# Optimization experiments

Measured on AMD Instinct MI355X. Metric: run time of the kernel, lower is better.

The kernel has to match this reference:

```python
import jax, jax.numpy as jnp
import numpy as np

B, N, S, K = 8, 4096, 1024, 16
C_IN, C_OUT = 128, 256
BN_EPS = 1e-5


def setup_inputs() -> dict:
    key = jax.random.key(0)
    ks = jax.random.split(key, 20)
    sc = 0.02
    p = {
        'xyz': jax.random.normal(ks[0], (B, N, 3), jnp.float32),
        'points': jax.random.normal(ks[1], (B, N, C_IN), jnp.float32),
        'wq': jax.random.normal(ks[2], (C_IN, C_OUT), jnp.float32) * sc,
        'wk': jax.random.normal(ks[3], (C_IN, C_OUT), jnp.float32) * sc,
        'wv': jax.random.normal(ks[4], (C_IN, C_OUT), jnp.float32) * sc,
        'dw1': jax.random.normal(ks[5], (3, C_OUT), jnp.float32) * sc,
        'db1': jnp.zeros((C_OUT,), jnp.float32),
        'dw2': jax.random.normal(ks[6], (C_OUT, C_OUT), jnp.float32) * sc,
        'db2': jnp.zeros((C_OUT,), jnp.float32),
        'gw1': jax.random.normal(ks[7], (C_OUT, C_OUT), jnp.float32) * sc,
        'gb1': jnp.zeros((C_OUT,), jnp.float32),
        'gw2': jax.random.normal(ks[8], (C_OUT, C_OUT), jnp.float32) * sc,
        'gb2': jnp.zeros((C_OUT,), jnp.float32),
        'lw': jax.random.normal(ks[9], (C_OUT, C_OUT), jnp.float32) * sc,
        'lb': jnp.zeros((C_OUT,), jnp.float32),
        'bn_g': jnp.ones((C_OUT,), jnp.float32),
        'bn_b': jnp.zeros((C_OUT,), jnp.float32),
    }
    return p


def _fps(xyz, npoint):
    # xyz: [N,3] -> farthest point sample indices [npoint] (deterministic start at 0,
    # matching torch impl with fixed seed semantics)
    n = xyz.shape[0]
    def step(carry, _):
        dist, far = carry
        centroid = xyz[far]                      # [3]
        d = jnp.sum((xyz - centroid) ** 2, -1)   # [N]
        dist = jnp.minimum(dist, d)
        return (dist, jnp.argmax(dist).astype(jnp.int32)), far
    init = (jnp.full((n,), 1e10, xyz.dtype), jnp.int32(0))
    _, idx = jax.lax.scan(step, init, None, length=npoint)
    return idx  # [npoint]


def _mlp2(x, w1, b1, w2, b2):
    return jax.nn.relu(x @ w1 + b1) @ w2 + b2


def reference(xyz, points, wq, wk, wv, dw1, db1, dw2, db2,
              gw1, gb1, gw2, gb2, lw, lb, bn_g, bn_b):
    # --- sample_and_group (FPS + KNN, knn=True) ---
    fps_idx = jax.vmap(lambda x: _fps(x, S))(xyz)                 # [B,S]
    new_xyz = jnp.take_along_axis(xyz, fps_idx[..., None], 1)     # [B,S,3]
    # squared distances sampled->all: [B,S,N]
    d2 = (jnp.sum(new_xyz**2, -1)[:, :, None]
          - 2.0 * jnp.einsum('bsc,bnc->bsn', new_xyz, xyz)
          + jnp.sum(xyz**2, -1)[:, None, :])
    knn_idx = jax.lax.top_k(-d2, K)[1]                            # [B,S,K]
    gather = jax.vmap(lambda a, i: a[i])
    knn_xyz = gather(xyz, knn_idx)                                # [B,S,K,3]
    knn_xyz_norm = knn_xyz - new_xyz[:, :, None]                  # centered coords
    knn_points = gather(points, knn_idx)                          # [B,S,K,C_in]
    sampled_points = jnp.take_along_axis(points, fps_idx[..., None], 1)  # [B,S,C_in]

    # --- vector attention ---
    q = sampled_points @ wq                                       # [B,S,C_out]
    k = knn_points @ wk                                           # [B,S,K,C_out]
    v = knn_points @ wv                                           # [B,S,K,C_out]
    pos_enc = _mlp2(knn_xyz_norm, dw1, db1, dw2, db2)             # [B,S,K,C_out]
    att = _mlp2(q[:, :, None] - k + pos_enc, gw1, gb1, gw2, gb2)  # [B,S,K,C_out]
    att = jax.nn.softmax(att / np.sqrt(C_OUT).astype(np.float32), axis=-2)
    res = jnp.einsum('bmnf,bmnf->bmf', att, v + pos_enc)          # [B,S,C_out]

    # --- fc_last + BatchNorm1d (training-mode batch stats, biased var) + ReLU ---
    res = res @ lw + lb
    mean = jnp.mean(res, axis=(0, 1))
    var = jnp.var(res, axis=(0, 1))
    res = bn_g * (res - mean) * jax.lax.rsqrt(var + BN_EPS) + bn_b
    res = jax.nn.relu(res)
    return new_xyz, res
```

## Files before the change

### kernel.cpp

```cpp
#include <hip/hip_runtime.h>

typedef unsigned long long ull;
typedef __attribute__((ext_vector_type(8))) short bf16x8;
typedef __attribute__((ext_vector_type(4))) float f32x4;

__device__ __forceinline__ unsigned short bf16b(float x){
    unsigned u = __float_as_uint(x);
    unsigned r = (u + 0x7FFFu + ((u >> 16) & 1u)) >> 16;
    return (unsigned short)r;
}
__device__ __forceinline__ float b2f(unsigned short u){
    return __uint_as_float(((unsigned)u) << 16);
}
__device__ __forceinline__ void st4(unsigned short* p, f32x4 v){
    ull pk = (ull)bf16b(v[0]) | (((ull)bf16b(v[1])) << 16)
           | (((ull)bf16b(v[2])) << 32) | (((ull)bf16b(v[3])) << 48);
    *(ull*)p = pk;
}
__device__ __forceinline__ f32x4 ld4(const unsigned short* p){
    ull pk = *(const ull*)p;
    f32x4 v;
    v[0] = b2f((unsigned short)pk);
    v[1] = b2f((unsigned short)(pk >> 16));
    v[2] = b2f((unsigned short)(pk >> 32));
    v[3] = b2f((unsigned short)(pk >> 48));
    return v;
}

#define DPPMAX(k, ctrl) do { \
    unsigned _lo = (unsigned)(k), _hi = (unsigned)((k) >> 32); \
    unsigned _l2 = (unsigned)__builtin_amdgcn_update_dpp((int)_lo, (int)_lo, (ctrl), 0xF, 0xF, false); \
    unsigned _h2 = (unsigned)__builtin_amdgcn_update_dpp((int)_hi, (int)_hi, (ctrl), 0xF, 0xF, false); \
    ull _k2 = (((ull)_h2) << 32) | _l2; \
    if (_k2 > (k)) (k) = _k2; \
} while (0)
#define DPPMIN(k, ctrl) do { \
    unsigned _lo = (unsigned)(k), _hi = (unsigned)((k) >> 32); \
    unsigned _l2 = (unsigned)__builtin_amdgcn_update_dpp((int)_lo, (int)_lo, (ctrl), 0xF, 0xF, false); \
    unsigned _h2 = (unsigned)__builtin_amdgcn_update_dpp((int)_hi, (int)_hi, (ctrl), 0xF, 0xF, false); \
    ull _k2 = (((ull)_h2) << 32) | _l2; \
    if (_k2 < (k)) (k) = _k2; \
} while (0)

template<int KT>
__device__ __forceinline__ int swz(int r, int c){
    return r * (KT * 32) + ((((c >> 3) + r) & (KT * 4 - 1)) << 3) + (c & 7);
}

template<int KT>
__device__ __forceinline__ void gemmT(const unsigned short* __restrict__ Wt,
                                      const unsigned short* __restrict__ Blds,
                                      int ch0, int lane, f32x4 acc[4][4])
{
    int i = lane & 15, q = lane >> 4;
#pragma unroll
    for (int kt = 0; kt < KT; kt++){
        int k0 = kt * 32 + q * 8;
        bf16x8 bfr[4], afr[4];
#pragma unroll
        for (int nt = 0; nt < 4; nt++)
            bfr[nt] = *(const bf16x8*)(Blds + swz<KT>(nt * 16 + i, k0));
#pragma unroll
        for (int mt = 0; mt < 4; mt++)
            afr[mt] = *(const bf16x8*)(Wt + (size_t)(ch0 + mt * 16 + i) * (KT * 32) + k0);
#pragma unroll
        for (int mt = 0; mt < 4; mt++)
#pragma unroll
            for (int nt = 0; nt < 4; nt++)
                acc[mt][nt] = __builtin_amdgcn_mfma_f32_16x16x32_bf16(afr[mt], bfr[nt], acc[mt][nt], 0, 0, 0);
    }
}

#define ZERO44(A) do { _Pragma("unroll") for (int _m = 0; _m < 4; _m++) \
    { _Pragma("unroll") for (int _n = 0; _n < 4; _n++) { A[_m][_n][0]=0.f;A[_m][_n][1]=0.f;A[_m][_n][2]=0.f;A[_m][_n][3]=0.f; } } } while(0)

#define CTRL_AUX   (8 << 4)

__device__ __forceinline__ int ald(const int* p){
    return __hip_atomic_load(p, __ATOMIC_RELAXED, __HIP_MEMORY_SCOPE_AGENT);
}
__device__ __forceinline__ void ast(int* p, int v){
    __hip_atomic_store(p, v, __ATOMIC_RELAXED, __HIP_MEMORY_SCOPE_AGENT);
}

__device__ __forceinline__ void knn_one(int t2, int G, float qx, float qy, float qz,
        const float* __restrict__ xyz,
        int* __restrict__ knn_idx, float* d2s, ull* kslot)
{
    int b = G >> 10;
    int lane = t2 & 63, wvi = t2 >> 6;
    float qq = qx * qx + qy * qy + qz * qz;
    for (int j = 0; j < 16; j++){
        int p = t2 + (j << 8);
        const float* s = xyz + ((size_t)b * 4096 + p) * 3;
        float x = s[0], y = s[1], z = s[2];
        d2s[p] = qq - 2.f * (qx * x + qy * y + qz * z) + (x * x + y * y + z * z);
    }
    __syncthreads();
    for (int r = 0; r < 16; r++){
        ull best = ~0ull;
#pragma unroll
        for (int j = 0; j < 16; j++){
            int p = t2 + (j << 8);
            unsigned bb = __float_as_uint(d2s[p]);
            bb = (bb & 0x80000000u) ? ~bb : (bb | 0x80000000u);
            ull key = (((ull)bb) << 32) | (unsigned)p;
            if (key < best) best = key;
        }
        DPPMIN(best, 0xB1); DPPMIN(best, 0x4E); DPPMIN(best, 0x141);
        DPPMIN(best, 0x140); DPPMIN(best, 0x142); DPPMIN(best, 0x143);
        if (lane == 63) kslot[wvi] = best;
        __syncthreads();
        if (t2 == 0){
            ull bk = kslot[0];
            for (int w = 1; w < 4; w++) if (kslot[w] < bk) bk = kslot[w];
            int p = (int)(unsigned)bk;
            knn_idx[(size_t)G * 16 + r] = p;
            d2s[p] = 3.0e38f;
        }
        __syncthreads();
    }
}

__device__ void attn_unit(int t, char* base, int G0, const float* nxL4,
    const unsigned short* __restrict__ pts16,
    const float* __restrict__ xyz,
    const int* __restrict__ knn_idx, const float* __restrict__ qbuf,
    const unsigned short* __restrict__ wkT, const unsigned short* __restrict__ wvT,
    const unsigned short* __restrict__ dw2T, const unsigned short* __restrict__ gw1T,
    const unsigned short* __restrict__ gw2T,
    const float* __restrict__ dw1, const float* __restrict__ db1,
    const float* __restrict__ db2, const float* __restrict__ gb1, const float* __restrict__ gb2,
    unsigned short* __restrict__ resY)
{
    unsigned short* bufA = (unsigned short*)base;
    unsigned short* bufU = (unsigned short*)(base + 32768);
    int lane = t & 63, wave = t >> 6;
    int i = lane & 15, q = lane >> 4;
    int ch0 = wave * 64;
    unsigned short* ptsA = bufU;
    float* dw1s  = (float*)(bufU + 8192);
    float* db1s  = (float*)(bufU + 9728);
    float* xyznS = (float*)(bufU + 10240);
    int*   idxs  = (int*)  (bufU + 10624);

    if (t < 64) idxs[t] = knn_idx[G0 * 16 + t];
    dw1s[t] = dw1[t]; dw1s[256 + t] = dw1[256 + t]; dw1s[512 + t] = dw1[512 + t];
    db1s[t] = db1[t];
    __syncthreads();

    if (t < 64){
        int G = G0 + (t >> 4); int bb = G >> 10; int p = idxs[t];
        const float* xp = xyz + ((size_t)bb * 4096 + p) * 3;
        const float* nz = nxL4 + (t >> 4) * 3;
        xyznS[t * 3 + 0] = xp[0] - nz[0];
        xyznS[t * 3 + 1] = xp[1] - nz[1];
        xyznS[t * 3 + 2] = xp[2] - nz[2];
    }
    {
        int r = t >> 2, seg = t & 3;
        int G = G0 + (r >> 4); int bb = G >> 10; int p = idxs[r];
        const uint4* src = (const uint4*)(pts16 + ((size_t)bb * 4096 + p) * 128 + seg * 32);
#pragma unroll
        for (int j = 0; j < 4; j++){
            uint4 v = src[j];
            *(uint4*)(ptsA + swz<4>(r, seg * 32 + j * 8)) = v;
        }
    }
    __syncthreads();

    {
        int r = lane;
        int o0 = wave * 64;
        float x = xyznS[r * 3], y = xyznS[r * 3 + 1], z = xyznS[r * 3 + 2];
#pragma unroll
        for (int j = 0; j < 64; j += 4){
            int o = o0 + j;
            f32x4 v;
#pragma unroll
            for (int e = 0; e < 4; e++)
                v[e] = fmaxf(db1s[o + e] + x * dw1s[o + e] + y * dw1s[256 + o + e] + z * dw1s[512 + o + e], 0.f);
            st4(bufA + swz<8>(r, o), v);
        }
    }
    __syncthreads();

    f32x4 accP[4][4]; ZERO44(accP);
    gemmT<8>(dw2T, bufA, ch0, lane, accP);
#pragma unroll
    for (int mt = 0; mt < 4; mt++){
        f32x4 d2v = *(const f32x4*)(db2 + ch0 + mt * 16 + q * 4);
#pragma unroll
        for (int nt = 0; nt < 4; nt++) accP[mt][nt] += d2v;
    }
    f32x4 accK[4][4]; ZERO44(accK);
    gemmT<4>(wkT, ptsA, ch0, lane, accK);
    __syncthreads();

#pragma unroll
    for (int mt = 0; mt < 4; mt++){
        int c = ch0 + mt * 16 + q * 4;
#pragma unroll
        for (int nt = 0; nt < 4; nt++){
            int r = nt * 16 + i;
            f32x4 qv = *(const f32x4*)(qbuf + (size_t)(G0 + nt) * 256 + c);
            f32x4 tv = qv - accK[mt][nt] + accP[mt][nt];
            st4(bufA + swz<8>(r, c), tv);
        }
    }
    f32x4 accV[4][4]; ZERO44(accV);
    gemmT<4>(wvT, ptsA, ch0, lane, accV);
    __syncthreads();

#pragma unroll
    for (int mt = 0; mt < 4; mt++){
        int c = ch0 + mt * 16 + q * 4;
#pragma unroll
        for (int nt = 0; nt < 4; nt++){
            int r = nt * 16 + i;
            f32x4 uv = accV[mt][nt] + accP[mt][nt];
            st4(bufU + swz<8>(r, c), uv);
        }
    }
    f32x4 acc1[4][4]; ZERO44(acc1);
    gemmT<8>(gw1T, bufA, ch0, lane, acc1);
    __syncthreads();

#pragma unroll
    for (int mt = 0; mt < 4; mt++){
        int c = ch0 + mt * 16 + q * 4;
        f32x4 g1v = *(const f32x4*)(gb1 + c);
#pragma unroll
        for (int nt = 0; nt < 4; nt++){
            int r = nt * 16 + i;
            f32x4 av = acc1[mt][nt] + g1v;
#pragma unroll
            for (int e = 0; e < 4; e++) av[e] = fmaxf(av[e], 0.f);
            st4(bufA + swz<8>(r, c), av);
        }
    }
    __syncthreads();

    f32x4 acc2[4][4]; ZERO44(acc2);
    gemmT<8>(gw2T, bufA, ch0, lane, acc2);
    __syncthreads();

#pragma unroll
    for (int mt = 0; mt < 4; mt++){
        int c = ch0 + mt * 16 + q * 4;
        f32x4 g2v = *(const f32x4*)(gb2 + c);
#pragma unroll
        for (int nt = 0; nt < 4; nt++){
            int r = nt * 16 + i;
            f32x4 ev;
#pragma unroll
            for (int e = 0; e < 4; e++) ev[e] = __expf((acc2[mt][nt][e] + g2v[e]) * 0.0625f);
            st4(bufA + swz<8>(r, c), ev);
        }
    }
    __syncthreads();

    {
        int g = t >> 6, c4 = (t & 63) * 4;
        f32x4 num; num[0]=0.f;num[1]=0.f;num[2]=0.f;num[3]=0.f;
        f32x4 den = num;
#pragma unroll
        for (int rr = 0; rr < 16; rr++){
            int r = g * 16 + rr;
            f32x4 e4 = ld4(bufA + swz<8>(r, c4));
            f32x4 u4 = ld4(bufU + swz<8>(r, c4));
            num += e4 * u4;
            den += e4;
        }
        f32x4 rv = num / den;
        st4(resY + (size_t)(G0 + g) * 256 + c4, rv);
    }
}

__device__ void do_chunk(int t, int c, char* SM,
    const float* __restrict__ xyz, const float* __restrict__ nxyz,
    const float* __restrict__ points, const float* __restrict__ wqT,
    const int* __restrict__ fps_idx, int* __restrict__ knn_idx, float* __restrict__ qbuf,
    const unsigned short* __restrict__ pts16,
    const unsigned short* __restrict__ wkT, const unsigned short* __restrict__ wvT,
    const unsigned short* __restrict__ dw2T, const unsigned short* __restrict__ gw1T,
    const unsigned short* __restrict__ gw2T,
    const float* __restrict__ dw1, const float* __restrict__ db1,
    const float* __restrict__ db2, const float* __restrict__ gb1, const float* __restrict__ gb2,
    unsigned short* __restrict__ resY)
{
    int g0 = c * 8;
    int sub = t >> 8, t2 = t & 255;
    int*   fpsL = (int*)  (SM + 131200);
    float* nxL  = (float*)(SM + 131232);
    if (t < 64){
        for (;;){
            int v = 0; bool ok = true;
            if (t < 8){
                v = ald(fps_idx + g0 + t); ok = (v != -1);
            } else if (t < 32){
                v = ald((const int*)nxyz + (size_t)g0 * 3 + (t - 8)); ok = (v != (int)0xFFFFFFFF);
            }
            if (__ballot(ok) == ~0ull){
                if (t < 8) fpsL[t] = v;
                else if (t < 32) ((int*)nxL)[t - 8] = v;
                break;
            }
            __builtin_amdgcn_s_sleep(8);
        }
    }
    __syncthreads();
    float* d2s = (float*)(SM + sub * 16384);
    ull* kslot = (ull*)(SM + 131072) + sub * 4;
    for (int r4 = 0; r4 < 4; r4++){
        int gl = r4 * 2 + sub;
        knn_one(t2, g0 + gl, nxL[gl * 3], nxL[gl * 3 + 1], nxL[gl * 3 + 2],
                xyz, knn_idx, d2s, kslot);
    }
    __syncthreads();
    {
        float* sp = (float*)SM;
        if (t < 256){
            int r = t >> 5, c4 = (t & 31) * 4;
            int G = g0 + r; int b = G >> 10; int p = fpsL[r];
            *(f32x4*)(sp + r * 128 + c4) = *(const f32x4*)(points + ((size_t)b * 4096 + p) * 128 + c4);
        }
        __syncthreads();
        float acc[4] = {0.f, 0.f, 0.f, 0.f};
        const float* wr = wqT + t2 * 128;
        for (int k = 0; k < 128; k += 4){
            f32x4 w = *(const f32x4*)(wr + k);
#pragma unroll
            for (int r = 0; r < 4; r++){
                const float* row = sp + (sub * 4 + r) * 128;
                acc[r] += w[0]*row[k] + w[1]*row[k+1] + w[2]*row[k+2] + w[3]*row[k+3];
            }
        }
#pragma unroll
        for (int r = 0; r < 4; r++) qbuf[(size_t)(g0 + sub * 4 + r) * 256 + t2] = acc[r];
        __syncthreads();
    }
    attn_unit(t2, SM + sub * 65536, g0 + sub * 4, nxL + sub * 12, pts16, xyz, knn_idx, qbuf,
              wkT, wvT, dw2T, gw1T, gw2T, dw1, db1, db2, gb1, gb2, resY);
    __syncthreads();
}

__global__ __launch_bounds__(256) void init_ws(int* __restrict__ ctrl,
                                               int* __restrict__ fps_idx,
                                               int* __restrict__ nxyz_i)
{
    int i = blockIdx.x * 256 + threadIdx.x;
    if (i < 256) ctrl[i] = 0;
    if (i < 8192) fps_idx[i] = -1;
    if (i < 24576) nxyz_i[i] = (int)0xFFFFFFFF;
}

__global__ __launch_bounds__(512, 2) void mega(
    const float* __restrict__ xyz, float* __restrict__ nxyz_out, int* __restrict__ fps_idx,
    const float* __restrict__ pts, unsigned short* __restrict__ pts16,
    const float* __restrict__ wq, const float* __restrict__ wk, const float* __restrict__ wv,
    const float* __restrict__ dw2, const float* __restrict__ gw1, const float* __restrict__ gw2,
    const float* __restrict__ lw,
    float* __restrict__ wqT, unsigned short* __restrict__ wkT, unsigned short* __restrict__ wvT,
    unsigned short* __restrict__ dw2T, unsigned short* __restrict__ gw1T,
    unsigned short* __restrict__ gw2T, unsigned short* __restrict__ lwT,
    float* __restrict__ stats,
    const float* __restrict__ dw1, const float* __restrict__ db1, const float* __restrict__ db2,
    const float* __restrict__ gb1, const float* __restrict__ gb2,
    int* __restrict__ knn_idx, float* __restrict__ qbuf, unsigned short* __restrict__ resY,
    int* __restrict__ ctrl)
{
    __shared__ __align__(16) char SM[132096];
    int blk = blockIdx.x, t = threadIdx.x;

    if (blk < 8){
        int b = blk;
        int lane = t & 63, wvi = t >> 6;
        float* sx = (float*)SM;
        float* sy = (float*)(SM + 16384);
        float* sz = (float*)(SM + 32768);
        int* farS = (int*)(SM + 49152);
        ull (*slotK)[8] = (ull(*)[8])(SM + 53248);
        for (int p = t; p < 4096; p += 512){
            const float* s = xyz + ((size_t)b * 4096 + p) * 3;
            sx[p] = s[0]; sy[p] = s[1]; sz[p] = s[2];
        }
        __syncthreads();
        float px[8], py[8], pz[8], dist[8];
        unsigned nplo[8];
#pragma unroll
        for (int j = 0; j < 8; j++){
            int p = t + (j << 9);
            px[j] = sx[p]; py[j] = sy[p]; pz[j] = sz[p];
            dist[j] = 1e10f;
            nplo[j] = ~(unsigned)p;
            asm volatile("" : "+v"(px[j]), "+v"(py[j]), "+v"(pz[j]), "+v"(nplo[j]));
        }
        int far = 0;
        float cx = sx[0], cy = sy[0], cz = sz[0];
        int par = 0;
        for (int s = 0; s < 1024; s++){
            if (t == 0) farS[s] = far;
            ull lb = 0;
#pragma unroll
            for (int j = 0; j < 8; j++){
                float dx = __fsub_rn(px[j], cx);
                float dy = __fsub_rn(py[j], cy);
                float dz = __fsub_rn(pz[j], cz);
                float d = __fadd_rn(__fadd_rn(__fmul_rn(dx, dx), __fmul_rn(dy, dy)), __fmul_rn(dz, dz));
                float nd = fminf(dist[j], d);
                dist[j] = nd;
                ull k2 = (((ull)__float_as_uint(nd)) << 32) | nplo[j];
                if (k2 > lb) lb = k2;
            }
            DPPMAX(lb, 0xB1); DPPMAX(lb, 0x4E); DPPMAX(lb, 0x141);
            DPPMAX(lb, 0x140); DPPMAX(lb, 0x142); DPPMAX(lb, 0x143);
            if (lane == 63) slotK[par][wvi] = lb;
            __syncthreads();
            ull k = slotK[par][lane & 7];
            DPPMAX(k, 0xB1); DPPMAX(k, 0x4E); DPPMAX(k, 0x141);
            far = (int)(~(unsigned)k);
            cx = sx[far]; cy = sy[far]; cz = sz[far];
            if (((s & 15) == 15) && wvi == 7){
                int s0 = s - 15;
                if (lane < 16){
                    ast(fps_idx + b * 1024 + s0 + lane, farS[s0 + lane]);
                } else {
                    int idx = lane - 16;
                    int st = s0 + idx / 3, d = idx - (idx / 3) * 3;
                    int f = farS[st];
                    float v = (d == 0) ? sx[f] : ((d == 1) ? sy[f] : sz[f]);
                    ast((int*)nxyz_out + (size_t)b * 3072 + st * 3 + d, __float_as_int(v));
                }
            }
            par ^= 1;
        }
        if (t == 0){ while (ald(ctrl + CTRL_AUX) < 248) __builtin_amdgcn_s_sleep(16); }
        __syncthreads();
        __threadfence();
        do_chunk(t, b * 128 + 127, SM, xyz, nxyz_out, pts, wqT, fps_idx, knn_idx, qbuf,
                 pts16, wkT, wvT, dw2T, gw1T, gw2T, dw1, db1, db2, gb1, gb2, resY);
        return;
    }

    int w = blk - 8;
    for (int base = w; base < 704; base += 248){
        if (base == 0) stats[t & 511] = 0.f;
        int i = base * 512 + t;
        if (i < 32768){ int n = i >> 7, kk = i & 127; wqT[i] = wq[kk * 256 + n]; }
        else if (i < 65536){ int j = i - 32768; int n = j >> 7, kk = j & 127; wkT[j] = bf16b(wk[kk * 256 + n]); }
        else if (i < 98304){ int j = i - 65536; int n = j >> 7, kk = j & 127; wvT[j] = bf16b(wv[kk * 256 + n]); }
        else if (i < 163840){ int j = i - 98304; int n = j >> 8, kk = j & 255; dw2T[j] = bf16b(dw2[kk * 256 + n]); }
        else if (i < 229376){ int j = i - 163840; int n = j >> 8, kk = j & 255; gw1T[j] = bf16b(gw1[kk * 256 + n]); }
        else if (i < 294912){ int j = i - 229376; int n = j >> 8, kk = j & 255; gw2T[j] = bf16b(gw2[kk * 256 + n]); }
        else { int j = i - 294912; int n = j >> 8, kk = j & 255; lwT[j] = bf16b(lw[kk * 256 + n]); }
    }
    for (int base = w; base < 2048; base += 248){
        int i = (base * 512 + t) * 4;
        f32x4 v = *(const f32x4*)(pts + i);
        ull pk = (ull)bf16b(v[0]) | (((ull)bf16b(v[1])) << 16)
               | (((ull)bf16b(v[2])) << 32) | (((ull)bf16b(v[3])) << 48);
        *(ull*)(pts16 + i) = pk;
    }
    __threadfence();
    __syncthreads();
    if (t == 0){
        atomicAdd(ctrl + CTRL_AUX, 1);
        while (ald(ctrl + CTRL_AUX) < 248) __builtin_amdgcn_s_sleep(16);
    }
    __syncthreads();
    __threadfence();
    for (int j = 0; j < 5; j++){
        int p = w + 248 * j;
        if (p >= 1016) break;
        int bb = p & 7, cc = p >> 3;
        do_chunk(t, bb * 128 + cc, SM, xyz, nxyz_out, pts, wqT, fps_idx, knn_idx, qbuf,
                 pts16, wkT, wvT, dw2T, gw1T, gw2T, dw1, db1, db2, gb1, gb2, resY);
    }
}

__global__ __launch_bounds__(256, 2) void z_gemm(const unsigned short* __restrict__ resY,
                                                 const unsigned short* __restrict__ lwT,
                                                 const float* __restrict__ lb,
                                                 float* __restrict__ zbuf,
                                                 float* __restrict__ stats)
{
    int t = threadIdx.x, lane = t & 63, wave = t >> 6;
    int i = lane & 15, q = lane >> 4;
    int row0 = blockIdx.x * 128;
    int ch0 = wave * 64;
    f32x4 acc[4][8];
#pragma unroll
    for (int mt = 0; mt < 4; mt++)
#pragma unroll
        for (int nt = 0; nt < 8; nt++){ acc[mt][nt][0]=0.f;acc[mt][nt][1]=0.f;acc[mt][nt][2]=0.f;acc[mt][nt][3]=0.f; }
#pragma unroll
    for (int kt = 0; kt < 8; kt++){
        int k0 = kt * 32 + q * 8;
        bf16x8 a[4], bb[8];
#pragma unroll
        for (int mt = 0; mt < 4; mt++)
            a[mt] = *(const bf16x8*)(lwT + (size_t)(ch0 + mt * 16 + i) * 256 + k0);
#pragma unroll
        for (int nt = 0; nt < 8; nt++)
            bb[nt] = *(const bf16x8*)(resY + (size_t)(row0 + nt * 16 + i) * 256 + k0);
#pragma unroll
        for (int mt = 0; mt < 4; mt++)
#pragma unroll
            for (int nt = 0; nt < 8; nt++)
                acc[mt][nt] = __builtin_amdgcn_mfma_f32_16x16x32_bf16(a[mt], bb[nt], acc[mt][nt], 0, 0, 0);
    }
    f32x4 s1[4], s2[4];
#pragma unroll
    for (int mt = 0; mt < 4; mt++){ s1[mt][0]=0.f;s1[mt][1]=0.f;s1[mt][2]=0.f;s1[mt][3]=0.f; s2[mt]=s1[mt]; }
#pragma unroll
    for (int mt = 0; mt < 4; mt++){
        int c = ch0 + mt * 16 + q * 4;
        f32x4 lb4 = *(const f32x4*)(lb + c);
#pragma unroll
        for (int nt = 0; nt < 8; nt++){
            int r = row0 + nt * 16 + i;
            f32x4 z = acc[mt][nt] + lb4;
            *(f32x4*)(zbuf + (size_t)r * 256 + c) = z;
            s1[mt] += z;
            s2[mt] += z * z;
        }
    }
    for (int m = 1; m < 16; m <<= 1){
#pragma unroll
        for (int mt = 0; mt < 4; mt++)
#pragma unroll
            for (int e = 0; e < 4; e++){
                s1[mt][e] += __shfl_xor(s1[mt][e], m);
                s2[mt][e] += __shfl_xor(s2[mt][e], m);
            }
    }
    if (i == 0){
#pragma unroll
        for (int mt = 0; mt < 4; mt++){
            int c = ch0 + mt * 16 + q * 4;
#pragma unroll
            for (int e = 0; e < 4; e++){
                atomicAdd(&stats[c + e], s1[mt][e]);
                atomicAdd(&stats[256 + c + e], s2[mt][e]);
            }
        }
    }
}

__global__ __launch_bounds__(256) void bn_kernel(const float* __restrict__ zbuf,
                                                 const float* __restrict__ stats,
                                                 const float* __restrict__ bn_g,
                                                 const float* __restrict__ bn_b,
                                                 float* __restrict__ out)
{
    int G = blockIdx.x, c = threadIdx.x;
    float mean = stats[c] * (1.f / 8192.f);
    float var = stats[256 + c] * (1.f / 8192.f) - mean * mean;
    float inv = rsqrtf(var + 1e-5f);
    float z = zbuf[(size_t)G * 256 + c];
    float y = bn_g[c] * (z - mean) * inv + bn_b[c];
    out[24576 + (size_t)G * 256 + c] = fmaxf(y, 0.f);
}

extern "C" void kernel_launch(void* const* d_in, const int* in_sizes, int n_in,
                              void* d_out, int out_size, void* d_ws, size_t ws_size,
                              hipStream_t stream)
{
    const float* xyz    = (const float*)d_in[0];
    const float* points = (const float*)d_in[1];
    const float* wq  = (const float*)d_in[2];
    const float* wk  = (const float*)d_in[3];
    const float* wv  = (const float*)d_in[4];
    const float* dw1 = (const float*)d_in[5];
    const float* db1 = (const float*)d_in[6];
    const float* dw2 = (const float*)d_in[7];
    const float* db2 = (const float*)d_in[8];
    const float* gw1 = (const float*)d_in[9];
    const float* gb1 = (const float*)d_in[10];
    const float* gw2 = (const float*)d_in[11];
    const float* gb2 = (const float*)d_in[12];
    const float* lw  = (const float*)d_in[13];
    const float* lb  = (const float*)d_in[14];
    const float* bn_g = (const float*)d_in[15];
    const float* bn_b = (const float*)d_in[16];
    float* out = (float*)d_out;

    char* ws = (char*)d_ws;
    int*            fps_idx = (int*)(ws + 0);
    int*            knn_idx = (int*)(ws + 32768);
    float*          qbuf    = (float*)(ws + 557056);
    unsigned short* pts16   = (unsigned short*)(ws + 8945664);
    unsigned short* wkT     = (unsigned short*)(ws + 17334272);
    unsigned short* wvT     = (unsigned short*)(ws + 17399808);
    unsigned short* dw2T    = (unsigned short*)(ws + 17465344);
    unsigned short* gw1T    = (unsigned short*)(ws + 17596416);
    unsigned short* gw2T    = (unsigned short*)(ws + 17727488);
    unsigned short* lwT     = (unsigned short*)(ws + 17858560);
    float*          wqT     = (float*)(ws + 17989632);
    unsigned short* resY    = (unsigned short*)(ws + 18120704);
    float*          zbuf    = (float*)(ws + 22315008);
    float*          stats   = (float*)(ws + 30703616);
    int*            ctrl    = (int*)(ws + 22315008);

    init_ws<<<96, 256, 0, stream>>>(ctrl, fps_idx, (int*)out);
    mega<<<256, 512, 0, stream>>>(xyz, out, fps_idx, points, pts16,
                                  wq, wk, wv, dw2, gw1, gw2, lw,
                                  wqT, wkT, wvT, dw2T, gw1T, gw2T, lwT, stats,
                                  dw1, db1, db2, gb1, gb2,
                                  knn_idx, qbuf, resY, ctrl);
    z_gemm<<<64, 256, 0, stream>>>(resY, lwT, lb, zbuf, stats);
    bn_kernel<<<8192, 256, 0, stream>>>(zbuf, stats, bn_g, bn_b, out);
}
```

Measured before the change: 926.4 us.

## Keep KNN distances in registers and double-buffer wave-min slots to halve barriers

The KNN top-16 selection now keeps each thread's 16 candidate distance keys in registers instead of shared memory. It also caches a per-thread local minimum that only the owning thread recomputes after its point is selected. Every thread reduces the four per-wave minima itself, and the slots alternate between two buffers, so one of the two block barriers per selection round is dropped. This cuts LDS traffic and repeated 16-element rescans, at the cost of more registers and a wider kslot region (8 entries per sub-group, 128 bytes total) that must not overlap fpsL at offset 131200.

```diff
diff --git a/kernel.cpp b/kernel.cpp
--- a/kernel.cpp
+++ b/kernel.cpp
@@ -85,40 +85,52 @@
 
 __device__ __forceinline__ void knn_one(int t2, int G, float qx, float qy, float qz,
         const float* __restrict__ xyz,
-        int* __restrict__ knn_idx, float* d2s, ull* kslot)
+        int* __restrict__ knn_idx, ull* kslot )
 {
     int b = G >> 10;
     int lane = t2 & 63, wvi = t2 >> 6;
     float qq = qx * qx + qy * qy + qz * qz;
+    unsigned fb[16];
+#pragma unroll
     for (int j = 0; j < 16; j++){
         int p = t2 + (j << 8);
         const float* s = xyz + ((size_t)b * 4096 + p) * 3;
         float x = s[0], y = s[1], z = s[2];
-        d2s[p] = qq - 2.f * (qx * x + qy * y + qz * z) + (x * x + y * y + z * z);
-    }
-    __syncthreads();
+        float d2 = qq - 2.f * (qx * x + qy * y + qz * z) + (x * x + y * y + z * z);
+        unsigned bb = __float_as_uint(d2);
+        fb[j] = (bb & 0x80000000u) ? ~bb : (bb | 0x80000000u);
+    }
+    ull lk = ~0ull;
+#pragma unroll
+    for (int j = 0; j < 16; j++){
+        ull key = (((ull)fb[j]) << 32) | (unsigned)(t2 + (j << 8));
+        if (key < lk) lk = key;
+    }
+    int par = 0;
     for (int r = 0; r < 16; r++){
-        ull best = ~0ull;
-#pragma unroll
-        for (int j = 0; j < 16; j++){
-            int p = t2 + (j << 8);
-            unsigned bb = __float_as_uint(d2s[p]);
-            bb = (bb & 0x80000000u) ? ~bb : (bb | 0x80000000u);
-            ull key = (((ull)bb) << 32) | (unsigned)p;
-            if (key < best) best = key;
-        }
-        DPPMIN(best, 0xB1); DPPMIN(best, 0x4E); DPPMIN(best, 0x141);
-        DPPMIN(best, 0x140); DPPMIN(best, 0x142); DPPMIN(best, 0x143);
-        if (lane == 63) kslot[wvi] = best;
+        ull k = lk;
+        DPPMIN(k, 0xB1); DPPMIN(k, 0x4E); DPPMIN(k, 0x141);
+        DPPMIN(k, 0x140); DPPMIN(k, 0x142); DPPMIN(k, 0x143);
+        if (lane == 63) kslot[par * 4 + wvi] = k;
         __syncthreads();
-        if (t2 == 0){
-            ull bk = kslot[0];
-            for (int w = 1; w < 4; w++) if (kslot[w] < bk) bk = kslot[w];
-            int p = (int)(unsigned)bk;
+        ull s0 = kslot[par * 4 + 0], s1 = kslot[par * 4 + 1];
+        ull s2 = kslot[par * 4 + 2], s3 = kslot[par * 4 + 3];
+        ull ga = s0 < s1 ? s0 : s1;
+        ull gb = s2 < s3 ? s2 : s3;
+        ull g  = ga < gb ? ga : gb;
+        int p = (int)(unsigned)g;
+        if (t2 == (p & 255)){
             knn_idx[(size_t)G * 16 + r] = p;
-            d2s[p] = 3.0e38f;
-        }
-        __syncthreads();
+            int jw = p >> 8;
+            lk = ~0ull;
+#pragma unroll
+            for (int j = 0; j < 16; j++){
+                if (j == jw) fb[j] = 0xFFFFFFFFu;
+                ull key = (((ull)fb[j]) << 32) | (unsigned)(t2 + (j << 8));
+                if (key < lk) lk = key;
+            }
+        }
+        par ^= 1;
     }
 }
 
@@ -291,8 +303,9 @@
 {
     int g0 = c * 8;
     int sub = t >> 8, t2 = t & 255;
-    int*   fpsL = (int*)  (SM + 131200);
-    float* nxL  = (float*)(SM + 131232);
+    ull*   kslot = (ull*)(SM + 131072) + sub * 8;
+    int*   fpsL  = (int*)  (SM + 131200);
+    float* nxL   = (float*)(SM + 131232);
     if (t < 64){
         for (;;){
             int v = 0; bool ok = true;
@@ -310,12 +323,10 @@
         }
     }
     __syncthreads();
-    float* d2s = (float*)(SM + sub * 16384);
-    ull* kslot = (ull*)(SM + 131072) + sub * 4;
     for (int r4 = 0; r4 < 4; r4++){
         int gl = r4 * 2 + sub;
         knn_one(t2, g0 + gl, nxL[gl * 3], nxL[gl * 3 + 1], nxL[gl * 3 + 2],
-                xyz, knn_idx, d2s, kslot);
+                xyz, knn_idx, kslot);
     }
     __syncthreads();
     {
```

Result: no change. 911.8 us (-1.6%).
